# Optimization experiments

Hardware: AMD Instinct MI355X
Metric: run time of the kernel (lower is better)

## Reference

```python
import jax, jax.numpy as jnp
import numpy as np
import math

B, C, N = 8, 128, 16384
H = 4
DK = C // H
COUT = 128
EPS = 1e-5

def _ln(x, g, b):
    # x: (B,H,N,DK); g,b: (H,DK) -> per-head LayerNorm over last dim
    mu = jnp.mean(x, axis=-1, keepdims=True)
    var = jnp.mean((x - mu) ** 2, axis=-1, keepdims=True)
    xh = (x - mu) / jnp.sqrt(var + EPS)
    return xh * g[None, :, None, :] + b[None, :, None, :]

def setup_inputs() -> dict:
    key = jax.random.key(0)
    ks = jax.random.split(key, 12)
    s = 0.02
    return {
        "x": jax.random.normal(ks[0], (B, C, N), jnp.float32),
        "Wq": jax.random.normal(ks[1], (C, C), jnp.float32) * s + 0.01 * jnp.eye(C),
        "bq": jnp.zeros((C,), jnp.float32),
        "Wk": jax.random.normal(ks[2], (C, C), jnp.float32) * s + 0.01 * jnp.eye(C),
        "bk": jnp.zeros((C,), jnp.float32),
        "Wv": jax.random.normal(ks[3], (C, C), jnp.float32) * s + 0.01 * jnp.eye(C),
        "bv": jnp.zeros((C,), jnp.float32),
        "gK": jnp.ones((H, DK), jnp.float32),
        "bK": jnp.zeros((H, DK), jnp.float32),
        "gV": jnp.ones((H, DK), jnp.float32),
        "bV": jnp.zeros((H, DK), jnp.float32),
        "Wo": jax.random.normal(ks[4], (COUT, C), jnp.float32) * s,
        "bo": jnp.zeros((COUT,), jnp.float32),
    }

def reference(x, Wq, bq, Wk, bk, Wv, bv, gK, bK, gV, bV, Wo, bo):
    # x: (B, C, N) -> (B, N, C)
    xt = jnp.transpose(x, (0, 2, 1))
    def proj(W, b):
        y = xt @ W.T + b                      # (B,N,C)
        return jnp.transpose(y.reshape(B, N, H, DK), (0, 2, 1, 3))  # (B,H,N,DK)
    q = proj(Wq, bq)
    k = proj(Wk, bk)
    v = proj(Wv, bv)
    # galerkin: per-head LayerNorm on K and V (vectorized over heads)
    k = _ln(k, gK, bK)
    v = _ln(v, gV, bV)
    # linear (no-softmax) attention: (Q K^T / sqrt(dk)) / N @ V == Q @ (K^T V) / (sqrt(dk)*N)
    # dropout from F.dropout is treated as identity (deterministic reference)
    kv = jnp.einsum("bhnd,bhne->bhde", k, v)            # (B,H,DK,DK)
    attn = jnp.einsum("bhnd,bhde->bhne", q, kv) / (math.sqrt(DK) * N)
    out = jnp.transpose(attn, (0, 2, 1, 3)).reshape(B, N, C)  # merge heads
    out = out @ Wo.T + bo                                # (B,N,COUT)
    return jnp.transpose(out, (0, 2, 1))                 # (B,COUT,N)
```

## Files before the change

kernel.cpp:

```cpp
#include <hip/hip_runtime.h>
#include <cmath>

#define BB 8
#define CC 128
#define NN 16384
#define HH 4
#define NBK 64
#define SX 272

typedef __attribute__((ext_vector_type(8))) short bf16x8;
typedef __attribute__((ext_vector_type(4))) float f32x4;

#define MFMA(a, b, c) __builtin_amdgcn_mfma_f32_16x16x32_bf16(a, b, c, 0, 0, 0)

__device__ __forceinline__ unsigned short f2b(float f) {
  union { float f; unsigned u; } v; v.f = f;
  unsigned r = v.u + 0x7FFFu + ((v.u >> 16) & 1u);
  return (unsigned short)(r >> 16);
}

__device__ __forceinline__ int xt_addr(int n, int cblk) {
  return n * SX + ((cblk ^ ((n >> 2) & 7)) << 4);
}
__device__ __forceinline__ int kt_byte(int c, int n) {
  return c * 144 + ((((n >> 3) ^ (c & 7)) << 4) | ((n & 7) << 1));
}

__global__ void k_prep(const float* __restrict__ Wq, const float* __restrict__ Wk,
                       const float* __restrict__ Wv, const float* __restrict__ Wo,
                       unsigned short* __restrict__ Wb) {
  const int idx = blockIdx.x * 256 + threadIdx.x;
  const int which = idx >> 14;
  const float* src = (which == 0) ? Wq : (which == 1) ? Wk : (which == 2) ? Wv : Wo;
  Wb[idx] = f2b(src[idx & 16383]);
}

__global__ __launch_bounds__(512, 4)
void k_fuse1(const float* __restrict__ x,
             const unsigned short* __restrict__ Wkb, const unsigned short* __restrict__ Wvb,
             const float* __restrict__ bk, const float* __restrict__ bv,
             const float* __restrict__ gK, const float* __restrict__ bK,
             const float* __restrict__ gV, const float* __restrict__ bV,
             float* __restrict__ kvp) {
  extern __shared__ char lds[];
  char* XT = lds;
  char* KT = lds + 34816;
  char* VT = lds + 53248;
  float* KVS = (float*)lds;

  const int tid = threadIdx.x;
  const int lane = tid & 63;
  const int w = tid >> 6;
  const int b = blockIdx.y;
  const int bx = blockIdx.x;
  const int l15 = lane & 15, l4 = lane >> 4;

  const int ph = w >> 1, pp = w & 1;
  const int kh = w >> 1, khalf = w & 1;

  const unsigned short* Wsrc = pp ? Wvb : Wkb;
  bf16x8 wf[2][4];
#pragma unroll
  for (int mf = 0; mf < 2; ++mf)
#pragma unroll
    for (int ks = 0; ks < 4; ++ks)
      wf[mf][ks] = *(const bf16x8*)(Wsrc + (ph * 32 + mf * 16 + l15) * 128 + ks * 32 + l4 * 8);

  float bias[2][4], gam[2][4], bet[2][4];
  {
    const float* bsrc = pp ? bv : bk;
    const float* gsrc = pp ? gV : gK;
    const float* esrc = pp ? bV : bK;
#pragma unroll
    for (int mf = 0; mf < 2; ++mf)
#pragma unroll
      for (int r = 0; r < 4; ++r) {
        const int cg = ph * 32 + mf * 16 + l4 * 4 + r;
        bias[mf][r] = bsrc[cg]; gam[mf][r] = gsrc[cg]; bet[mf][r] = esrc[cg];
      }
  }

  f32x4 kvacc[2][2];
#pragma unroll
  for (int i = 0; i < 2; ++i)
#pragma unroll
    for (int j = 0; j < 2; ++j) kvacc[i][j] = (f32x4){0.f, 0.f, 0.f, 0.f};

  for (int ot = 0; ot < 2; ++ot) {
    const int n0 = (bx * 2 + ot) * 128;

#pragma unroll
    for (int g = 0; g < 2; ++g) {
      const int cb = w * 2 + g;
      const float* xb = x + ((size_t)b * CC + cb * 8) * NN + n0 + lane * 2;
      float2 va[8];
#pragma unroll
      for (int cc = 0; cc < 8; ++cc) va[cc] = *(const float2*)(xb + (size_t)cc * NN);
#pragma unroll
      for (int j = 0; j < 2; ++j) {
        const int n = lane * 2 + j;
        bf16x8 pk;
#pragma unroll
        for (int cc = 0; cc < 8; ++cc)
          ((unsigned short*)&pk)[cc] = f2b(j ? va[cc].y : va[cc].x);
        *(bf16x8*)(XT + n * SX + ((cb ^ ((n >> 2) & 7)) << 4)) = pk;
      }
    }
    __syncthreads();

    for (int t = 0; t < 2; ++t) {
      const int nbase = t * 64;
      char* DST = pp ? VT : KT;
#pragma unroll
      for (int nf = 0; nf < 4; ++nf) {
        const int n = nbase + nf * 16 + l15;
        f32x4 a0 = (f32x4){0.f, 0.f, 0.f, 0.f}, a1 = (f32x4){0.f, 0.f, 0.f, 0.f};
#pragma unroll
        for (int ks = 0; ks < 4; ++ks) {
          const bf16x8 xf = *(const bf16x8*)(XT + xt_addr(n, ks * 4 + l4));
          a0 = MFMA(wf[0][ks], xf, a0);
          a1 = MFMA(wf[1][ks], xf, a1);
        }
#pragma unroll
        for (int r = 0; r < 4; ++r) { a0[r] += bias[0][r]; a1[r] += bias[1][r]; }
        float s = 0.f, ss = 0.f;
#pragma unroll
        for (int r = 0; r < 4; ++r) {
          s += a0[r] + a1[r];
          ss += a0[r] * a0[r] + a1[r] * a1[r];
        }
        s += __shfl_xor(s, 16); ss += __shfl_xor(ss, 16);
        s += __shfl_xor(s, 32); ss += __shfl_xor(ss, 32);
        const float mu = s * (1.f / 32.f);
        const float var = ss * (1.f / 32.f) - mu * mu;
        const float rstd = rsqrtf(var + 1e-5f);
        const int nloc = nf * 16 + l15;
#pragma unroll
        for (int r = 0; r < 4; ++r) {
          const int c0k = ph * 32 + l4 * 4 + r;
          *(unsigned short*)(DST + kt_byte(c0k, nloc)) =
              f2b((a0[r] - mu) * rstd * gam[0][r] + bet[0][r]);
          const int c1k = ph * 32 + 16 + l4 * 4 + r;
          *(unsigned short*)(DST + kt_byte(c1k, nloc)) =
              f2b((a1[r] - mu) * rstd * gam[1][r] + bet[1][r]);
        }
      }
      __syncthreads();

#pragma unroll
      for (int mf = 0; mf < 2; ++mf) {
        const int ck = kh * 32 + mf * 16 + l15;
        const bf16x8 ka = *(const bf16x8*)(KT + ck * 144 + (((khalf * 4 + l4) ^ (ck & 7)) << 4));
#pragma unroll
        for (int ef = 0; ef < 2; ++ef) {
          const int cv = kh * 32 + ef * 16 + l15;
          const bf16x8 vb = *(const bf16x8*)(VT + cv * 144 + (((khalf * 4 + l4) ^ (cv & 7)) << 4));
          kvacc[mf][ef] = MFMA(ka, vb, kvacc[mf][ef]);
        }
      }
      __syncthreads();
    }
  }

#pragma unroll
  for (int mf = 0; mf < 2; ++mf)
#pragma unroll
    for (int ef = 0; ef < 2; ++ef)
#pragma unroll
      for (int r = 0; r < 4; ++r) {
        const int d = mf * 16 + l4 * 4 + r, e = ef * 16 + l15;
        KVS[w * 1024 + d * 32 + e] = kvacc[mf][ef][r];
      }
  __syncthreads();
  {
    float* og = kvp + ((size_t)(b * NBK + bx)) * 8192;
#pragma unroll
    for (int i = 0; i < 4; ++i) {
      const int off = i * 2048 + tid * 4;
      *(f32x4*)(og + off) = *(const f32x4*)(KVS + off);
    }
  }
}

__global__ void k_reduceA(const float* __restrict__ kvp, float* __restrict__ p2) {
  const int blk = blockIdx.x;
  const int s = blk & 7, h = (blk >> 3) & 3, b = blk >> 5;
  const int t = threadIdx.x;
  f32x4 acc = (f32x4){0.f, 0.f, 0.f, 0.f};
  for (int i = 0; i < 8; ++i) {
    const int bx = s * 8 + i;
    const float* base = kvp + ((size_t)(b * NBK + bx)) * 8192 + t * 4;
    acc += *(const f32x4*)(base + (2 * h) * 1024);
    acc += *(const f32x4*)(base + (2 * h + 1) * 1024);
  }
  *(f32x4*)(p2 + (size_t)blk * 1024 + t * 4) = acc;
}

__global__ void k_reduceB(const float* __restrict__ p2, unsigned short* __restrict__ kvT,
                          const float scale) {
  const int bh = blockIdx.x;
  const int t = threadIdx.x;
  f32x4 acc = (f32x4){0.f, 0.f, 0.f, 0.f};
  for (int s = 0; s < 8; ++s)
    acc += *(const f32x4*)(p2 + ((size_t)bh * 8 + s) * 1024 + t * 4);
#pragma unroll
  for (int j = 0; j < 4; ++j) {
    const int i = t * 4 + j;
    const int d = i >> 5, e = i & 31;
    kvT[(size_t)bh * 1024 + e * 32 + d] = f2b(acc[j] * scale);
  }
}

__global__ __launch_bounds__(512, 4)
void k_pass2(const float* __restrict__ x,
             const unsigned short* __restrict__ Wqb, const float* __restrict__ bq,
             const unsigned short* __restrict__ kvT,
             const unsigned short* __restrict__ Wob, const float* __restrict__ bo,
             float* __restrict__ out) {
  extern __shared__ char lds[];
  char* QS = lds + 34816;
  char* AS = lds + 51200;

  const int tid = threadIdx.x;
  const int lane = tid & 63;
  const int w = tid >> 6;
  const int b = blockIdx.y;
  const int l15 = lane & 15, l4 = lane >> 4;
  const int h = w >> 1, half = w & 1;

  bf16x8 kvf[2];
#pragma unroll
  for (int mf = 0; mf < 2; ++mf)
    kvf[mf] = *(const bf16x8*)(kvT + (((size_t)b * HH + h) * 32 + mf * 16 + l15) * 32 + l4 * 8);
  bf16x8 wq[4], wo[4];
#pragma unroll
  for (int ks = 0; ks < 4; ++ks) {
    wq[ks] = *(const bf16x8*)(Wqb + (w * 16 + l15) * 128 + ks * 32 + l4 * 8);
    wo[ks] = *(const bf16x8*)(Wob + (w * 16 + l15) * 128 + ks * 32 + l4 * 8);
  }
  float bq_r[4], bo_r[4];
#pragma unroll
  for (int r = 0; r < 4; ++r) {
    bq_r[r] = bq[w * 16 + l4 * 4 + r];
    bo_r[r] = bo[w * 16 + l4 * 4 + r];
  }

  const int half2 = lane >> 5;
  const int cb2 = w * 2 + half2;
  const int nn = (lane & 31) * 2;
  const float* xrow = x + ((size_t)b * CC + cb2 * 8) * NN + blockIdx.x * 256 + nn;
  float* ob = out + (size_t)b * CC * NN;

  float2 rx[8];
#pragma unroll
  for (int cc = 0; cc < 8; ++cc) rx[cc] = *(const float2*)(xrow + (size_t)cc * NN);

  for (int it = 0; it < 4; ++it) {
    const int n0 = blockIdx.x * 256 + it * 64;
    char* XT = (it & 1) ? (lds + 17408) : lds;

#pragma unroll
    for (int j = 0; j < 2; ++j) {
      const int n = nn + j;
      bf16x8 pk;
#pragma unroll
      for (int cc = 0; cc < 8; ++cc)
        ((unsigned short*)&pk)[cc] = f2b(j ? rx[cc].y : rx[cc].x);
      *(bf16x8*)(XT + n * SX + ((cb2 ^ ((n >> 2) & 7)) << 4)) = pk;
    }
    if (it < 3) {
      const float* xn = xrow + (it + 1) * 64;
#pragma unroll
      for (int cc = 0; cc < 8; ++cc) rx[cc] = *(const float2*)(xn + (size_t)cc * NN);
    }
    __syncthreads();

    f32x4 qa[4];
#pragma unroll
    for (int nf = 0; nf < 4; ++nf) qa[nf] = (f32x4){0.f, 0.f, 0.f, 0.f};
#pragma unroll
    for (int ks = 0; ks < 4; ++ks)
#pragma unroll
      for (int nf = 0; nf < 4; ++nf) {
        const int n = nf * 16 + l15;
        const bf16x8 xf = *(const bf16x8*)(XT + xt_addr(n, ks * 4 + l4));
        qa[nf] = MFMA(wq[ks], xf, qa[nf]);
      }
#pragma unroll
    for (int nf = 0; nf < 4; ++nf) {
      const int n = nf * 16 + l15;
      const int c0 = w * 16 + l4 * 4;
      unsigned long long pk = 0;
#pragma unroll
      for (int r = 0; r < 4; ++r)
        pk |= (unsigned long long)f2b(qa[nf][r] + bq_r[r]) << (16 * r);
      *(unsigned long long*)(QS + n * 256 + (((c0 >> 3) ^ (n & 15)) << 4) + ((c0 & 7) << 1)) = pk;
    }
    __syncthreads();

    f32x4 aa[2][2];
#pragma unroll
    for (int i = 0; i < 2; ++i)
#pragma unroll
      for (int j = 0; j < 2; ++j) aa[i][j] = (f32x4){0.f, 0.f, 0.f, 0.f};
    bf16x8 qf[2];
#pragma unroll
    for (int nf = 0; nf < 2; ++nf) {
      const int n = half * 32 + nf * 16 + l15;
      const int cq = h * 32 + l4 * 8;
      qf[nf] = *(const bf16x8*)(QS + n * 256 + ((((cq >> 3)) ^ (n & 15)) << 4));
    }
#pragma unroll
    for (int mf = 0; mf < 2; ++mf)
#pragma unroll
      for (int nf = 0; nf < 2; ++nf) aa[mf][nf] = MFMA(kvf[mf], qf[nf], aa[mf][nf]);
#pragma unroll
    for (int mf = 0; mf < 2; ++mf)
#pragma unroll
      for (int nf = 0; nf < 2; ++nf) {
        const int n = half * 32 + nf * 16 + l15;
        const int e0 = h * 32 + mf * 16 + l4 * 4;
        unsigned long long pk = 0;
#pragma unroll
        for (int r = 0; r < 4; ++r)
          pk |= (unsigned long long)f2b(aa[mf][nf][r]) << (16 * r);
        *(unsigned long long*)(AS + n * 256 + (((e0 >> 3) ^ (n & 15)) << 4) + ((e0 & 7) << 1)) = pk;
      }
    __syncthreads();

    f32x4 oa[4];
#pragma unroll
    for (int nf = 0; nf < 4; ++nf) oa[nf] = (f32x4){0.f, 0.f, 0.f, 0.f};
#pragma unroll
    for (int ks = 0; ks < 4; ++ks)
#pragma unroll
      for (int nf = 0; nf < 4; ++nf) {
        const int n = nf * 16 + l15;
        const bf16x8 af = *(const bf16x8*)(AS + n * 256 + (((ks * 4 + l4) ^ (n & 15)) << 4));
        oa[nf] = MFMA(wo[ks], af, oa[nf]);
      }
#pragma unroll
    for (int nf = 0; nf < 4; ++nf)
#pragma unroll
      for (int r = 0; r < 4; ++r) {
        const int c = w * 16 + l4 * 4 + r;
        ob[(size_t)c * NN + n0 + nf * 16 + l15] = oa[nf][r] + bo_r[r];
      }
  }
}

extern "C" void kernel_launch(void* const* d_in, const int* in_sizes, int n_in,
                              void* d_out, int out_size, void* d_ws, size_t ws_size,
                              hipStream_t stream) {
  const float* x  = (const float*)d_in[0];
  const float* Wq = (const float*)d_in[1];
  const float* bq = (const float*)d_in[2];
  const float* Wk = (const float*)d_in[3];
  const float* bk = (const float*)d_in[4];
  const float* Wv = (const float*)d_in[5];
  const float* bv = (const float*)d_in[6];
  const float* gK = (const float*)d_in[7];
  const float* bK = (const float*)d_in[8];
  const float* gV = (const float*)d_in[9];
  const float* bV = (const float*)d_in[10];
  const float* Wo = (const float*)d_in[11];
  const float* bo = (const float*)d_in[12];
  float* out = (float*)d_out;

  char* ws = (char*)d_ws;
  float* kvp = (float*)ws;
  float* p2  = kvp + (size_t)BB * NBK * 8192;
  unsigned short* kvTb = (unsigned short*)(p2 + 256 * 1024);
  unsigned short* Wb = kvTb + (size_t)BB * HH * 1024;
  const unsigned short* Wqb = Wb;
  const unsigned short* Wkb = Wb + 16384;
  const unsigned short* Wvb = Wb + 32768;
  const unsigned short* Wob = Wb + 49152;

  (void)hipFuncSetAttribute(reinterpret_cast<const void*>(k_fuse1),
                            hipFuncAttributeMaxDynamicSharedMemorySize, 71680);
  (void)hipFuncSetAttribute(reinterpret_cast<const void*>(k_pass2),
                            hipFuncAttributeMaxDynamicSharedMemorySize, 67584);

  k_prep<<<256, 256, 0, stream>>>(Wq, Wk, Wv, Wo, Wb);

  k_fuse1<<<dim3(NBK, BB), 512, 71680, stream>>>(
      x, Wkb, Wvb, bk, bv, gK, bK, gV, bV, kvp);

  k_reduceA<<<256, 256, 0, stream>>>(kvp, p2);

  const float scale = 1.0f / (5.65685424949238f * 16384.0f);
  k_reduceB<<<32, 256, 0, stream>>>(p2, kvTb, scale);

  k_pass2<<<dim3(NBK, BB), 512, 67584, stream>>>(
      x, Wqb, bq, kvTb, Wob, bo, out);
}
```

Before: 73.50 us.

## Double k_fuse1 block size and merge two-stage KV reduction into one kernel

k_fuse1 now runs 1024-thread blocks over 256-column tiles, with two 8-wave halves each holding private K/V LDS buffers, and sums the two halves' KV partials in-block before writing. This halves the number of partial KV tiles. The two reduction kernels become a single k_reduce launch that sums 32 partials per (b,h). The goal is to cut a launch and reduce partial-sum traffic, at the cost of 140KB of LDS per block, which allows only one block per CU and may hurt latency hiding.

```diff
diff --git a/kernel.cpp b/kernel.cpp
--- a/kernel.cpp
+++ b/kernel.cpp
@@ -5,7 +5,8 @@
 #define CC 128
 #define NN 16384
 #define HH 4
-#define NBK 64
+#define NB1 32
+#define NB2 64
 #define SX 272
 
 typedef __attribute__((ext_vector_type(8))) short bf16x8;
@@ -35,7 +36,7 @@
   Wb[idx] = f2b(src[idx & 16383]);
 }
 
-__global__ __launch_bounds__(512, 4)
+__global__ __launch_bounds__(1024, 4)
 void k_fuse1(const float* __restrict__ x,
              const unsigned short* __restrict__ Wkb, const unsigned short* __restrict__ Wvb,
              const float* __restrict__ bk, const float* __restrict__ bv,
@@ -44,8 +45,7 @@
              float* __restrict__ kvp) {
   extern __shared__ char lds[];
   char* XT = lds;
-  char* KT = lds + 34816;
-  char* VT = lds + 53248;
+  char* KVB = lds + 69632;
   float* KVS = (float*)lds;
 
   const int tid = threadIdx.x;
@@ -55,8 +55,11 @@
   const int bx = blockIdx.x;
   const int l15 = lane & 15, l4 = lane >> 4;
 
-  const int ph = w >> 1, pp = w & 1;
-  const int kh = w >> 1, khalf = w & 1;
+  const int nh = w >> 3, rw = w & 7;
+  const int ph = rw >> 1, pp = rw & 1;
+  const int kh = rw >> 1, khalf = rw & 1;
+  char* KTn = KVB + nh * 18432;
+  char* VTn = KVB + 36864 + nh * 18432;
 
   const unsigned short* Wsrc = pp ? Wvb : Wkb;
   bf16x8 wf[2][4];
@@ -87,30 +90,28 @@
     for (int j = 0; j < 2; ++j) kvacc[i][j] = (f32x4){0.f, 0.f, 0.f, 0.f};
 
   for (int ot = 0; ot < 2; ++ot) {
-    const int n0 = (bx * 2 + ot) * 128;
-
-#pragma unroll
-    for (int g = 0; g < 2; ++g) {
-      const int cb = w * 2 + g;
-      const float* xb = x + ((size_t)b * CC + cb * 8) * NN + n0 + lane * 2;
-      float2 va[8];
-#pragma unroll
-      for (int cc = 0; cc < 8; ++cc) va[cc] = *(const float2*)(xb + (size_t)cc * NN);
-#pragma unroll
-      for (int j = 0; j < 2; ++j) {
-        const int n = lane * 2 + j;
+    const int n0 = (bx * 2 + ot) * 256;
+
+    {
+      const float* xb = x + ((size_t)b * CC + w * 8) * NN + n0 + lane * 4;
+      f32x4 va[8];
+#pragma unroll
+      for (int cc = 0; cc < 8; ++cc) va[cc] = *(const f32x4*)(xb + (size_t)cc * NN);
+#pragma unroll
+      for (int j = 0; j < 4; ++j) {
+        const int n = lane * 4 + j;
         bf16x8 pk;
 #pragma unroll
         for (int cc = 0; cc < 8; ++cc)
-          ((unsigned short*)&pk)[cc] = f2b(j ? va[cc].y : va[cc].x);
-        *(bf16x8*)(XT + n * SX + ((cb ^ ((n >> 2) & 7)) << 4)) = pk;
+          ((unsigned short*)&pk)[cc] = f2b(va[cc][j]);
+        *(bf16x8*)(XT + n * SX + ((w ^ ((n >> 2) & 7)) << 4)) = pk;
       }
     }
     __syncthreads();
 
     for (int t = 0; t < 2; ++t) {
-      const int nbase = t * 64;
-      char* DST = pp ? VT : KT;
+      const int nbase = nh * 128 + t * 64;
+      char* DST = pp ? VTn : KTn;
 #pragma unroll
       for (int nf = 0; nf < 4; ++nf) {
         const int n = nbase + nf * 16 + l15;
@@ -150,11 +151,11 @@
 #pragma unroll
       for (int mf = 0; mf < 2; ++mf) {
         const int ck = kh * 32 + mf * 16 + l15;
-        const bf16x8 ka = *(const bf16x8*)(KT + ck * 144 + (((khalf * 4 + l4) ^ (ck & 7)) << 4));
+        const bf16x8 ka = *(const bf16x8*)(KTn + ck * 144 + (((khalf * 4 + l4) ^ (ck & 7)) << 4));
 #pragma unroll
         for (int ef = 0; ef < 2; ++ef) {
           const int cv = kh * 32 + ef * 16 + l15;
-          const bf16x8 vb = *(const bf16x8*)(VT + cv * 144 + (((khalf * 4 + l4) ^ (cv & 7)) << 4));
+          const bf16x8 vb = *(const bf16x8*)(VTn + cv * 144 + (((khalf * 4 + l4) ^ (cv & 7)) << 4));
           kvacc[mf][ef] = MFMA(ka, vb, kvacc[mf][ef]);
         }
       }
@@ -173,42 +174,30 @@
       }
   __syncthreads();
   {
-    float* og = kvp + ((size_t)(b * NBK + bx)) * 8192;
-#pragma unroll
-    for (int i = 0; i < 4; ++i) {
-      const int off = i * 2048 + tid * 4;
-      *(f32x4*)(og + off) = *(const f32x4*)(KVS + off);
-    }
-  }
-}
-
-__global__ void k_reduceA(const float* __restrict__ kvp, float* __restrict__ p2) {
-  const int blk = blockIdx.x;
-  const int s = blk & 7, h = (blk >> 3) & 3, b = blk >> 5;
-  const int t = threadIdx.x;
-  f32x4 acc = (f32x4){0.f, 0.f, 0.f, 0.f};
-  for (int i = 0; i < 8; ++i) {
-    const int bx = s * 8 + i;
-    const float* base = kvp + ((size_t)(b * NBK + bx)) * 8192 + t * 4;
-    acc += *(const f32x4*)(base + (2 * h) * 1024);
-    acc += *(const f32x4*)(base + (2 * h + 1) * 1024);
-  }
-  *(f32x4*)(p2 + (size_t)blk * 1024 + t * 4) = acc;
-}
-
-__global__ void k_reduceB(const float* __restrict__ p2, unsigned short* __restrict__ kvT,
-                          const float scale) {
+    float* og = kvp + ((size_t)(b * NB1 + bx)) * 8192;
+#pragma unroll
+    for (int i = 0; i < 2; ++i) {
+      const int off = i * 4096 + tid * 4;
+      const f32x4 v0 = *(const f32x4*)(KVS + off);
+      const f32x4 v1 = *(const f32x4*)(KVS + off + 8192);
+      *(f32x4*)(og + off) = v0 + v1;
+    }
+  }
+}
+
+__global__ void k_reduce(const float* __restrict__ kvp, unsigned short* __restrict__ kvT,
+                         const float scale) {
   const int bh = blockIdx.x;
-  const int t = threadIdx.x;
-  f32x4 acc = (f32x4){0.f, 0.f, 0.f, 0.f};
-  for (int s = 0; s < 8; ++s)
-    acc += *(const f32x4*)(p2 + ((size_t)bh * 8 + s) * 1024 + t * 4);
-#pragma unroll
-  for (int j = 0; j < 4; ++j) {
-    const int i = t * 4 + j;
-    const int d = i >> 5, e = i & 31;
-    kvT[(size_t)bh * 1024 + e * 32 + d] = f2b(acc[j] * scale);
-  }
+  const int h = bh & 3, b = bh >> 2;
+  const int i = threadIdx.x;
+  const float* base = kvp + (size_t)b * NB1 * 8192 + i;
+  float acc = 0.f;
+  for (int bx = 0; bx < NB1; ++bx) {
+    acc += base[(size_t)bx * 8192 + (2 * h) * 1024];
+    acc += base[(size_t)bx * 8192 + (2 * h + 1) * 1024];
+  }
+  const int d = i >> 5, e = i & 31;
+  kvT[(size_t)bh * 1024 + e * 32 + d] = f2b(acc * scale);
 }
 
 __global__ __launch_bounds__(512, 4)
@@ -369,8 +358,7 @@
 
   char* ws = (char*)d_ws;
   float* kvp = (float*)ws;
-  float* p2  = kvp + (size_t)BB * NBK * 8192;
-  unsigned short* kvTb = (unsigned short*)(p2 + 256 * 1024);
+  unsigned short* kvTb = (unsigned short*)(ws + (size_t)BB * NB1 * 8192 * 4);
   unsigned short* Wb = kvTb + (size_t)BB * HH * 1024;
   const unsigned short* Wqb = Wb;
   const unsigned short* Wkb = Wb + 16384;
@@ -378,20 +366,18 @@
   const unsigned short* Wob = Wb + 49152;
 
   (void)hipFuncSetAttribute(reinterpret_cast<const void*>(k_fuse1),
-                            hipFuncAttributeMaxDynamicSharedMemorySize, 71680);
+                            hipFuncAttributeMaxDynamicSharedMemorySize, 143360);
   (void)hipFuncSetAttribute(reinterpret_cast<const void*>(k_pass2),
                             hipFuncAttributeMaxDynamicSharedMemorySize, 67584);
 
   k_prep<<<256, 256, 0, stream>>>(Wq, Wk, Wv, Wo, Wb);
 
-  k_fuse1<<<dim3(NBK, BB), 512, 71680, stream>>>(
+  k_fuse1<<<dim3(NB1, BB), 1024, 143360, stream>>>(
       x, Wkb, Wvb, bk, bv, gK, bK, gV, bV, kvp);
 
-  k_reduceA<<<256, 256, 0, stream>>>(kvp, p2);
-
   const float scale = 1.0f / (5.65685424949238f * 16384.0f);
-  k_reduceB<<<32, 256, 0, stream>>>(p2, kvTb, scale);
-
-  k_pass2<<<dim3(NBK, BB), 512, 67584, stream>>>(
+  k_reduce<<<32, 1024, 0, stream>>>(kvp, kvTb, scale);
+
+  k_pass2<<<dim3(NB2, BB), 512, 67584, stream>>>(
       x, Wqb, bq, kvTb, Wob, bo, out);
 }
```

After: 78.42 us. +6.7%, slower.

## Pre-transpose x to swizzled bf16 global buffer shared by both passes

Applied to the files above, without the earlier changes.

Adds a k_xpose kernel that converts x from fp32 channel-major into a bf16, padded, swizzled n-major layout in workspace, matching the LDS tile format. k_fuse1 and k_pass2 then fill their LDS tiles with straight contiguous 16-byte copies instead of strided fp32 loads followed by in-register conversion and transpose. Separately, k_fuse1 now sums the two warp partials per head before writing kvp, which halves kvp size and the reads in k_reduceA. The cost is an extra kernel launch plus a full read of x and a write of the roughly 35 MB bf16 copy, which the later passes then read back, possibly from the large last-level cache.

```diff
diff --git a/kernel.cpp b/kernel.cpp
--- a/kernel.cpp
+++ b/kernel.cpp
@@ -35,8 +35,39 @@
   Wb[idx] = f2b(src[idx & 16383]);
 }
 
+__global__ __launch_bounds__(1024)
+void k_xpose(const float* __restrict__ x, unsigned char* __restrict__ xTg) {
+  extern __shared__ char lds[];
+  const int tid = threadIdx.x;
+  const int lane = tid & 63;
+  const int w = tid >> 6;
+  const int b = blockIdx.y;
+  const int n0 = blockIdx.x * 512;
+
+#pragma unroll
+  for (int seg = 0; seg < 2; ++seg) {
+    const float* xb = x + ((size_t)b * CC + w * 8) * NN + n0 + seg * 256 + lane * 4;
+    f32x4 va[8];
+#pragma unroll
+    for (int cc = 0; cc < 8; ++cc) va[cc] = *(const f32x4*)(xb + (size_t)cc * NN);
+#pragma unroll
+    for (int j = 0; j < 4; ++j) {
+      const int n = seg * 256 + lane * 4 + j;
+      bf16x8 pk;
+#pragma unroll
+      for (int cc = 0; cc < 8; ++cc)
+        ((unsigned short*)&pk)[cc] = f2b(va[cc][j]);
+      *(bf16x8*)(lds + n * SX + ((w ^ ((n >> 2) & 7)) << 4)) = pk;
+    }
+  }
+  __syncthreads();
+  unsigned char* dst = xTg + ((size_t)b * NN + n0) * SX;
+  for (int off = tid * 16; off < 512 * SX; off += 16384)
+    *(float4*)(dst + off) = *(const float4*)(lds + off);
+}
+
 __global__ __launch_bounds__(512, 4)
-void k_fuse1(const float* __restrict__ x,
+void k_fuse1(const unsigned char* __restrict__ xTg,
              const unsigned short* __restrict__ Wkb, const unsigned short* __restrict__ Wvb,
              const float* __restrict__ bk, const float* __restrict__ bv,
              const float* __restrict__ gK, const float* __restrict__ bK,
@@ -89,22 +120,10 @@
   for (int ot = 0; ot < 2; ++ot) {
     const int n0 = (bx * 2 + ot) * 128;
 
-#pragma unroll
-    for (int g = 0; g < 2; ++g) {
-      const int cb = w * 2 + g;
-      const float* xb = x + ((size_t)b * CC + cb * 8) * NN + n0 + lane * 2;
-      float2 va[8];
-#pragma unroll
-      for (int cc = 0; cc < 8; ++cc) va[cc] = *(const float2*)(xb + (size_t)cc * NN);
-#pragma unroll
-      for (int j = 0; j < 2; ++j) {
-        const int n = lane * 2 + j;
-        bf16x8 pk;
-#pragma unroll
-        for (int cc = 0; cc < 8; ++cc)
-          ((unsigned short*)&pk)[cc] = f2b(j ? va[cc].y : va[cc].x);
-        *(bf16x8*)(XT + n * SX + ((cb ^ ((n >> 2) & 7)) << 4)) = pk;
-      }
+    {
+      const unsigned char* src = xTg + ((size_t)b * NN + n0) * SX;
+      for (int off = tid * 16; off < 128 * SX; off += 8192)
+        *(float4*)(XT + off) = *(const float4*)(src + off);
     }
     __syncthreads();
 
@@ -173,11 +192,14 @@
       }
   __syncthreads();
   {
-    float* og = kvp + ((size_t)(b * NBK + bx)) * 8192;
-#pragma unroll
-    for (int i = 0; i < 4; ++i) {
+    float* og = kvp + ((size_t)(b * NBK + bx)) * 4096;
+#pragma unroll
+    for (int i = 0; i < 2; ++i) {
       const int off = i * 2048 + tid * 4;
-      *(f32x4*)(og + off) = *(const f32x4*)(KVS + off);
+      const int h = off >> 10, q = off & 1023;
+      const f32x4 v0 = *(const f32x4*)(KVS + (2 * h) * 1024 + q);
+      const f32x4 v1 = *(const f32x4*)(KVS + (2 * h + 1) * 1024 + q);
+      *(f32x4*)(og + off) = v0 + v1;
     }
   }
 }
@@ -189,9 +211,7 @@
   f32x4 acc = (f32x4){0.f, 0.f, 0.f, 0.f};
   for (int i = 0; i < 8; ++i) {
     const int bx = s * 8 + i;
-    const float* base = kvp + ((size_t)(b * NBK + bx)) * 8192 + t * 4;
-    acc += *(const f32x4*)(base + (2 * h) * 1024);
-    acc += *(const f32x4*)(base + (2 * h + 1) * 1024);
+    acc += *(const f32x4*)(kvp + ((size_t)(b * NBK + bx)) * 4096 + h * 1024 + t * 4);
   }
   *(f32x4*)(p2 + (size_t)blk * 1024 + t * 4) = acc;
 }
@@ -212,7 +232,7 @@
 }
 
 __global__ __launch_bounds__(512, 4)
-void k_pass2(const float* __restrict__ x,
+void k_pass2(const unsigned char* __restrict__ xTg,
              const unsigned short* __restrict__ Wqb, const float* __restrict__ bq,
              const unsigned short* __restrict__ kvT,
              const unsigned short* __restrict__ Wob, const float* __restrict__ bo,
@@ -245,33 +265,16 @@
     bo_r[r] = bo[w * 16 + l4 * 4 + r];
   }
 
-  const int half2 = lane >> 5;
-  const int cb2 = w * 2 + half2;
-  const int nn = (lane & 31) * 2;
-  const float* xrow = x + ((size_t)b * CC + cb2 * 8) * NN + blockIdx.x * 256 + nn;
   float* ob = out + (size_t)b * CC * NN;
-
-  float2 rx[8];
-#pragma unroll
-  for (int cc = 0; cc < 8; ++cc) rx[cc] = *(const float2*)(xrow + (size_t)cc * NN);
 
   for (int it = 0; it < 4; ++it) {
     const int n0 = blockIdx.x * 256 + it * 64;
     char* XT = (it & 1) ? (lds + 17408) : lds;
 
-#pragma unroll
-    for (int j = 0; j < 2; ++j) {
-      const int n = nn + j;
-      bf16x8 pk;
-#pragma unroll
-      for (int cc = 0; cc < 8; ++cc)
-        ((unsigned short*)&pk)[cc] = f2b(j ? rx[cc].y : rx[cc].x);
-      *(bf16x8*)(XT + n * SX + ((cb2 ^ ((n >> 2) & 7)) << 4)) = pk;
-    }
-    if (it < 3) {
-      const float* xn = xrow + (it + 1) * 64;
-#pragma unroll
-      for (int cc = 0; cc < 8; ++cc) rx[cc] = *(const float2*)(xn + (size_t)cc * NN);
+    {
+      const unsigned char* src = xTg + ((size_t)b * NN + n0) * SX;
+      for (int off = tid * 16; off < 64 * SX; off += 8192)
+        *(float4*)(XT + off) = *(const float4*)(src + off);
     }
     __syncthreads();
 
@@ -369,14 +372,17 @@
 
   char* ws = (char*)d_ws;
   float* kvp = (float*)ws;
-  float* p2  = kvp + (size_t)BB * NBK * 8192;
+  float* p2  = kvp + (size_t)BB * NBK * 4096;
   unsigned short* kvTb = (unsigned short*)(p2 + 256 * 1024);
   unsigned short* Wb = kvTb + (size_t)BB * HH * 1024;
+  unsigned char* xT = (unsigned char*)(Wb + 65536);
   const unsigned short* Wqb = Wb;
   const unsigned short* Wkb = Wb + 16384;
   const unsigned short* Wvb = Wb + 32768;
   const unsigned short* Wob = Wb + 49152;
 
+  (void)hipFuncSetAttribute(reinterpret_cast<const void*>(k_xpose),
+                            hipFuncAttributeMaxDynamicSharedMemorySize, 139264);
   (void)hipFuncSetAttribute(reinterpret_cast<const void*>(k_fuse1),
                             hipFuncAttributeMaxDynamicSharedMemorySize, 71680);
   (void)hipFuncSetAttribute(reinterpret_cast<const void*>(k_pass2),
@@ -384,8 +390,10 @@
 
   k_prep<<<256, 256, 0, stream>>>(Wq, Wk, Wv, Wo, Wb);
 
+  k_xpose<<<dim3(NN / 512, BB), 1024, 139264, stream>>>(x, xT);
+
   k_fuse1<<<dim3(NBK, BB), 512, 71680, stream>>>(
-      x, Wkb, Wvb, bk, bv, gK, bK, gV, bV, kvp);
+      xT, Wkb, Wvb, bk, bv, gK, bK, gV, bV, kvp);
 
   k_reduceA<<<256, 256, 0, stream>>>(kvp, p2);
 
@@ -393,5 +401,5 @@
   k_reduceB<<<32, 256, 0, stream>>>(p2, kvTb, scale);
 
   k_pass2<<<dim3(NBK, BB), 512, 67584, stream>>>(
-      x, Wqb, bq, kvTb, Wob, bo, out);
-}
+      xT, Wqb, bq, kvTb, Wob, bo, out);
+}
```

Result: slower. 81.51 us (+10.9%).
